# Optimization experiments

Hardware: AMD Instinct MI355X
Metric: run time of the kernel (lower is better)

Reference implementation:

```python
import jax, jax.numpy as jnp
import numpy as np

IN_DIM = 128
SLOT_SIZE = 64
NUM_SLOTS = 8
NUM_ITERS = 3
MLP_HDIM = 128
EPSILON = 1e-08


def _layernorm(x, g, b, eps=1e-5):
    m = jnp.mean(x, axis=-1, keepdims=True)
    v = jnp.mean((x - m) ** 2, axis=-1, keepdims=True)
    return (x - m) * jax.lax.rsqrt(v + eps) * g + b


def setup_inputs() -> dict:
    key = jax.random.key(0)
    ks = jax.random.split(key, 16)
    H, D, K, M = SLOT_SIZE, IN_DIM, NUM_SLOTS, MLP_HDIM
    x = jax.random.normal(ks[0], (32, 4096, D), dtype=jnp.float32)
    noise = jax.random.normal(ks[1], (32, K, H), dtype=jnp.float32)
    s = lambda k, shape, fan_in: jax.random.normal(k, shape, jnp.float32) * (1.0 / np.sqrt(fan_in))
    return {
        'x': x,
        'noise': noise,
        'Wq': s(ks[2], (H, H), H),            # project_q (no bias)
        'Wk': s(ks[3], (H, D), D),            # project_k
        'Wv': s(ks[4], (H, D), D),            # project_v
        'ln_in_g': jnp.ones((D,), jnp.float32), 'ln_in_b': jnp.zeros((D,), jnp.float32),
        'ln_sl_g': jnp.ones((H,), jnp.float32), 'ln_sl_b': jnp.zeros((H,), jnp.float32),
        'ln_mlp_g': jnp.ones((H,), jnp.float32), 'ln_mlp_b': jnp.zeros((H,), jnp.float32),
        'gru_w_ih': s(ks[5], (3 * H, H), H),  # PyTorch GRUCell weight_ih (r,z,n)
        'gru_w_hh': s(ks[6], (3 * H, H), H),
        'gru_b_ih': jnp.zeros((3 * H,), jnp.float32),
        'gru_b_hh': jnp.zeros((3 * H,), jnp.float32),
        'mlp_w1': s(ks[7], (M, H), H), 'mlp_b1': jnp.zeros((M,), jnp.float32),
        'mlp_w2': s(ks[8], (H, M), M), 'mlp_b2': jnp.zeros((H,), jnp.float32),
        'slots_mu': jnp.tile(jnp.linspace(-1.0, 1.0, K, dtype=jnp.float32)[None, :, None], (1, 1, H)),
        'slots_logsigma': jnp.full((1, K, H), -1.0, dtype=jnp.float32),
    }


def reference(x, noise, Wq, Wk, Wv, ln_in_g, ln_in_b, ln_sl_g, ln_sl_b,
              ln_mlp_g, ln_mlp_b, gru_w_ih, gru_w_hh, gru_b_ih, gru_b_hh,
              mlp_w1, mlp_b1, mlp_w2, mlp_b2, slots_mu, slots_logsigma):
    B = x.shape[0]
    H, K = SLOT_SIZE, NUM_SLOTS
    xn = _layernorm(x, ln_in_g, ln_in_b)
    k = jnp.einsum('bnd,hd->bnh', xn, Wk)  # [B,N,H]
    v = jnp.einsum('bnd,hd->bnh', xn, Wv)

    scale = jax.nn.softplus(slots_logsigma) + 1e-05
    slots = slots_mu + scale * noise  # rsample, broadcast over batch -> [B,K,H]

    def step(slots):
        slots_prev = slots
        s = _layernorm(slots, ln_sl_g, ln_sl_b)
        q = jnp.einsum('bkh,gh->bkg', s, Wq)  # [B,K,H]
        scores = (H ** -0.5) * jnp.einsum('bnh,bkh->bnk', k, q)
        attn = jax.nn.softmax(scores, axis=-1) + EPSILON  # softmax over slots
        attn = attn / jnp.sum(attn, axis=1, keepdims=True)  # normalize over inputs
        updates = jnp.einsum('bnk,bnh->bkh', attn, v)
        # PyTorch GRUCell: gates ordered (r, z, n)
        u = updates.reshape(-1, H)
        h = slots_prev.reshape(-1, H)
        gx = u @ gru_w_ih.T + gru_b_ih
        gh = h @ gru_w_hh.T + gru_b_hh
        xr, xz, xn_ = jnp.split(gx, 3, axis=-1)
        hr, hz, hn = jnp.split(gh, 3, axis=-1)
        r = jax.nn.sigmoid(xr + hr)
        z = jax.nn.sigmoid(xz + hz)
        n = jnp.tanh(xn_ + r * hn)
        slots = ((1.0 - z) * n + z * h).reshape(B, K, H)
        slots = _layernorm(slots, ln_mlp_g, ln_mlp_b)
        mlp_out = jax.nn.relu(slots @ mlp_w1.T + mlp_b1) @ mlp_w2.T + mlp_b2
        return slots + mlp_out

    for _ in range(NUM_ITERS):
        slots = step(slots)
    return slots
```

## Files before the change

kernel.cpp:

```cpp
#include <hip/hip_runtime.h>

typedef __attribute__((ext_vector_type(8))) short s16x8;
typedef __attribute__((ext_vector_type(4))) float f32x4;

#define DEV static __device__ __forceinline__

DEV float b2f(unsigned short u){
  unsigned int i = ((unsigned int)u) << 16;
  float f; __builtin_memcpy(&f, &i, 4); return f;
}
DEV unsigned short f2b(float f){
  unsigned int i; __builtin_memcpy(&i, &f, 4);
  i = i + 0x7fffu + ((i >> 16) & 1u);
  return (unsigned short)(i >> 16);
}
DEV f32x4 mfma16(s16x8 a, s16x8 b, f32x4 c){
  return __builtin_amdgcn_mfma_f32_16x16x32_bf16(a, b, c, 0, 0, 0);
}
DEV s16x8 ld8f(const float* p){
  const float4* q4 = (const float4*)p;
  float4 a = q4[0], b = q4[1];
  s16x8 r;
  r[0]=(short)f2b(a.x); r[1]=(short)f2b(a.y); r[2]=(short)f2b(a.z); r[3]=(short)f2b(a.w);
  r[4]=(short)f2b(b.x); r[5]=(short)f2b(b.y); r[6]=(short)f2b(b.z); r[7]=(short)f2b(b.w);
  return r;
}

template<int C> DEV float dpp_addstep(float x){
  int y = __builtin_amdgcn_update_dpp(0, __builtin_bit_cast(int, x), C, 0xF, 0xF, true);
  return x + __builtin_bit_cast(float, y);
}
DEV float rsum16(float v){
  v = dpp_addstep<0xB1>(v);
  v = dpp_addstep<0x4E>(v);
  v = dpp_addstep<0x141>(v);
  v = dpp_addstep<0x140>(v);
  return v;
}

__global__ __launch_bounds__(256) void k_wpack(
    const float* __restrict__ Wk, const float* __restrict__ Wv,
    const float* __restrict__ wih, const float* __restrict__ whh,
    const float* __restrict__ w1, const float* __restrict__ w2,
    const float* __restrict__ Wq,
    unsigned short* __restrict__ wkb, unsigned short* __restrict__ wvb,
    unsigned short* __restrict__ wall)
{
  int t = blockIdx.x * 256 + threadIdx.x;
  int off = t * 4;
  const float* src; unsigned short* dst;
  if      (off <  8192){ src = Wk  + off;         dst = wkb  + off; }
  else if (off < 16384){ src = Wv  + off -  8192; dst = wvb  + off - 8192; }
  else if (off < 28672){ src = wih + off - 16384; dst = wall + off - 16384; }
  else if (off < 40960){ src = whh + off - 28672; dst = wall + off - 16384; }
  else if (off < 49152){ src = w1  + off - 40960; dst = wall + off - 16384; }
  else if (off < 57344){ src = w2  + off - 49152; dst = wall + off - 16384; }
  else                 { src = Wq  + off - 57344; dst = wall + off - 16384; }
  float4 v = *(const float4*)src;
  ushort4 o;
  o.x = f2b(v.x); o.y = f2b(v.y); o.z = f2b(v.z); o.w = f2b(v.w);
  *(ushort4*)dst = o;
}

__global__ __launch_bounds__(256, 4) void k_lnkv5(
    const float* __restrict__ x,
    const unsigned short* __restrict__ wkb,
    const unsigned short* __restrict__ wvb,
    const float* __restrict__ lg,
    const float* __restrict__ lb,
    unsigned short* __restrict__ kg,
    unsigned short* __restrict__ vt,
    const float* __restrict__ noise,
    const float* __restrict__ mu,
    const float* __restrict__ lsg,
    const float* __restrict__ gsl,
    const float* __restrict__ bsl,
    const float* __restrict__ Wq,
    float* __restrict__ slots,
    unsigned short* __restrict__ qws)
{
  __shared__ __align__(16) unsigned int xs[128 * 68];
  const int tid = threadIdx.x;
  const int w = tid >> 6, ln = tid & 63;
  const int m16 = ln & 15, q = ln >> 4;

  if (blockIdx.x >= 1024){
    unsigned short* st = (unsigned short*)xs;
    float (*redS)[4] = (float(*)[4])((char*)xs + 2304);
    float (*redQ)[4] = (float(*)[4])((char*)xs + 2560);
    const int bi = blockIdx.x - 1024;
    const int r0 = bi * 16;
    const int cw = w*16 + m16;

    float sl[4], s1[4], s2[4];
    #pragma unroll
    for (int rr = 0; rr < 4; ++rr){
      int row = r0 + q*4 + rr;
      int k = row & 7;
      float v = mu[k*64 + cw] + (log1pf(expf(lsg[k*64 + cw])) + 1e-5f) * noise[row*64 + cw];
      sl[rr] = v;
      slots[row*64 + cw] = v;
      s1[rr] = v; s2[rr] = v*v;
    }
    #pragma unroll
    for (int m = 1; m < 16; m <<= 1){
      #pragma unroll
      for (int rr = 0; rr < 4; ++rr){
        s1[rr] += __shfl_xor(s1[rr], m);
        s2[rr] += __shfl_xor(s2[rr], m);
      }
    }
    if (m16 == 0){
      #pragma unroll
      for (int rr = 0; rr < 4; ++rr){ redS[q*4+rr][w] = s1[rr]; redQ[q*4+rr][w] = s2[rr]; }
    }
    __syncthreads();
    {
      const float gs = gsl[cw], bs = bsl[cw];
      #pragma unroll
      for (int rr = 0; rr < 4; ++rr){
        f32x4 aS = *(const f32x4*)redS[q*4+rr];
        f32x4 aQ = *(const f32x4*)redQ[q*4+rr];
        float tS = aS[0]+aS[1]+aS[2]+aS[3];
        float tQ = aQ[0]+aQ[1]+aQ[2]+aQ[3];
        float mean = tS*(1.f/64.f);
        float var  = tQ*(1.f/64.f) - mean*mean;
        float rs = rsqrtf(var + 1e-5f);
        float sq = (sl[rr] - mean)*rs*gs + bs;
        st[(q*4+rr)*72 + cw] = f2b(sq);
      }
    }
    __syncthreads();
    {
      f32x4 acc = {0,0,0,0};
      #pragma unroll
      for (int ks = 0; ks < 2; ++ks){
        s16x8 a = *(const s16x8*)(st + m16*72 + ks*32 + q*8);
        acc = mfma16(a, ld8f(Wq + cw*64 + ks*32 + q*8), acc);
      }
      #pragma unroll
      for (int rr = 0; rr < 4; ++rr){
        int row = r0 + q*4 + rr;
        int bb_ = row >> 3, kk = row & 7;
        qws[(bb_*16 + kk)*64 + cw] = f2b(acc[rr] * 0.125f);
      }
      int b0 = bi * 2;
      ((unsigned int*)(qws + (b0*16 + 8)*64))[tid] = 0u;
      ((unsigned int*)(qws + ((b0+1)*16 + 8)*64))[tid] = 0u;
    }
    return;
  }

  const int b = blockIdx.x >> 5;
  const int nbase = (blockIdx.x & 31) << 7;
  const long rowg0 = (long)b * 4096 + nbase;

  {
    const int c = m16;
    const float4 gA = *(const float4*)(lg + c*4);
    const float4 gB = *(const float4*)(lg + 64 + c*4);
    const float4 bA = *(const float4*)(lb + c*4);
    const float4 bB = *(const float4*)(lb + 64 + c*4);
    const float* base = x + (rowg0 + w*32 + q)*128;

    float4 va[2], vb[2];
    va[0] = *(const float4*)(base + c*4);
    vb[0] = *(const float4*)(base + 64 + c*4);
    #pragma unroll
    for (int p = 0; p < 8; ++p){
      const int cur = p & 1, nxt = cur ^ 1;
      if (p < 7){
        va[nxt] = *(const float4*)(base + (p+1)*512 + c*4);
        vb[nxt] = *(const float4*)(base + (p+1)*512 + 64 + c*4);
      }
      float4 u = va[cur], t = vb[cur];
      float s1 = (u.x + u.y) + (u.z + u.w) + (t.x + t.y) + (t.z + t.w);
      float s2 = (u.x*u.x + u.y*u.y) + (u.z*u.z + u.w*u.w)
               + (t.x*t.x + t.y*t.y) + (t.z*t.z + t.w*t.w);
      s1 = rsum16(s1);
      s2 = rsum16(s2);
      float mean = s1 * (1.f/128.f);
      float var  = s2 * (1.f/128.f) - mean*mean;
      float rs = rsqrtf(var + 1e-5f);
      float y0 = (u.x - mean)*rs*gA.x + bA.x;
      float y1 = (u.y - mean)*rs*gA.y + bA.y;
      float y2 = (u.z - mean)*rs*gA.z + bA.z;
      float y3 = (u.w - mean)*rs*gA.w + bA.w;
      float y4 = (t.x - mean)*rs*gB.x + bB.x;
      float y5 = (t.y - mean)*rs*gB.y + bB.y;
      float y6 = (t.z - mean)*rs*gB.z + bB.z;
      float y7 = (t.w - mean)*rs*gB.w + bB.w;
      uint2 pkA, pkB;
      pkA.x = (unsigned int)f2b(y0) | ((unsigned int)f2b(y1) << 16);
      pkA.y = (unsigned int)f2b(y2) | ((unsigned int)f2b(y3) << 16);
      pkB.x = (unsigned int)f2b(y4) | ((unsigned int)f2b(y5) << 16);
      pkB.y = (unsigned int)f2b(y6) | ((unsigned int)f2b(y7) << 16);
      const int r = w*32 + p*4 + q;
      *(uint2*)&xs[r*68 + c*2] = pkA;
      *(uint2*)&xs[r*68 + 32 + c*2] = pkB;
    }
  }

  s16x8 bw[4][4];
  #pragma unroll
  for (int t = 0; t < 4; ++t)
    #pragma unroll
    for (int kb = 0; kb < 4; ++kb)
      bw[kb][t] = *(const s16x8*)(wkb + (t*16 + m16)*128 + kb*32 + q*8);

  __syncthreads();

  const f32x4 zf = {0.f, 0.f, 0.f, 0.f};

  #pragma unroll
  for (int mi = 0; mi < 2; ++mi){
    int n0 = (w*2 + mi) * 16;
    f32x4 acc[4];
    #pragma unroll
    for (int t = 0; t < 4; ++t) acc[t] = zf;
    #pragma unroll
    for (int kb = 0; kb < 4; ++kb){
      s16x8 af = *(const s16x8*)((const unsigned short*)(xs + (n0 + m16)*68) + kb*32 + q*8);
      #pragma unroll
      for (int t = 0; t < 4; ++t)
        acc[t] = mfma16(af, bw[kb][t], acc[t]);
    }
    #pragma unroll
    for (int t = 0; t < 4; ++t){
      int h = t*16 + m16;
      #pragma unroll
      for (int rr = 0; rr < 4; ++rr){
        long n = rowg0 + n0 + q*4 + rr;
        kg[n*64 + h] = f2b(acc[t][rr]);
      }
    }
  }

  #pragma unroll
  for (int t = 0; t < 4; ++t)
    #pragma unroll
    for (int kb = 0; kb < 4; ++kb)
      bw[kb][t] = *(const s16x8*)(wvb + (t*16 + m16)*128 + kb*32 + q*8);

  #pragma unroll
  for (int mi = 0; mi < 2; ++mi){
    int n0 = (w*2 + mi) * 16;
    f32x4 acc[4];
    #pragma unroll
    for (int t = 0; t < 4; ++t) acc[t] = zf;
    #pragma unroll
    for (int kb = 0; kb < 4; ++kb){
      s16x8 af = *(const s16x8*)((const unsigned short*)(xs + (n0 + m16)*68) + kb*32 + q*8);
      #pragma unroll
      for (int t = 0; t < 4; ++t)
        acc[t] = mfma16(af, bw[kb][t], acc[t]);
    }
    #pragma unroll
    for (int t = 0; t < 4; ++t){
      int h = t*16 + m16;
      unsigned int p0 = (unsigned int)f2b(acc[t][0]) | ((unsigned int)f2b(acc[t][1]) << 16);
      unsigned int p1 = (unsigned int)f2b(acc[t][2]) | ((unsigned int)f2b(acc[t][3]) << 16);
      uint2 pv; pv.x = p0; pv.y = p1;
      long off = ((long)b*64 + h)*4096 + nbase + n0 + q*4;
      *(uint2*)(vt + off) = pv;
    }
  }
}

__global__ __launch_bounds__(256) void k_attn3(
    const unsigned short* __restrict__ kg,
    const unsigned short* __restrict__ vt,
    const unsigned short* __restrict__ qws,
    const unsigned short* __restrict__ wall,
    const float* __restrict__ bih, const float* __restrict__ bhh,
    const float* __restrict__ b1p, const float* __restrict__ b2p,
    const float* __restrict__ gmlp, const float* __restrict__ bmlp,
    const float* __restrict__ gsl, const float* __restrict__ bsl,
    const float* __restrict__ Up_in, const float* __restrict__ Sp_in,
    float* __restrict__ Up_out, float* __restrict__ Sp_out,
    const float* __restrict__ slin, float* __restrict__ slout,
    int it)
{
  __shared__ float sc[256*17];
  __shared__ unsigned short aT[16*264];
  __shared__ unsigned short ut[16*72], ht[16*72], st[16*72], hid[16*136];
  __shared__ unsigned short qloc[16*72];
  __shared__ __align__(16) float redS[16][4];
  __shared__ __align__(16) float redQ[16][4];

  const int tid = threadIdx.x;
  const int w = tid >> 6, ln = tid & 63;
  const int m16 = ln & 15, q = ln >> 4;
  const int b = blockIdx.x >> 4;
  const int tile = blockIdx.x & 15;
  const int nbase = tile << 8;

  for (int i = tid; i < 8*264; i += 256) aT[8*264 + i] = 0;
  if (tid < 128){
    int row = 8 + (tid >> 4), c = (tid & 15)*4;
    ushort4 z4 = {0,0,0,0};
    *(ushort4*)&qloc[row*72 + c] = z4;
  }

  if (it == 0){
    if (tid < 128){
      int row = tid >> 4, c = (tid & 15)*4;
      *(ushort4*)&qloc[row*72 + c] = *(const ushort4*)(qws + (b*16 + row)*64 + c);
    }
  } else {
    const int r0 = (b >> 1) * 16;
    const int cw = w*16 + m16;
    const unsigned short* wihb = wall;
    const unsigned short* whhb = wall + 12288;
    const unsigned short* w1b  = wall + 24576;
    const unsigned short* w2b  = wall + 32768;
    const unsigned short* wqb  = wall + 40960;

    #pragma unroll
    for (int p = 0; p < 4; ++p){
      int row = p*4 + w;
      int g = r0 + row;
      int bb = g >> 3, sl = g & 7;
      const float* up  = Up_in + ((bb*16)*8 + sl)*64 + ln;
      const float* spp = Sp_in + (bb*16)*8 + sl;
      float usum = 0.f, ssum = 0.f;
      #pragma unroll
      for (int t = 0; t < 16; ++t){
        usum += up[t*512];
        ssum += spp[t*8];
      }
      ut[row*72 + ln] = f2b(usum / ssum);
      ht[row*72 + ln] = f2b(slin[g*64 + ln]);
    }
    __syncthreads();

    f32x4 axr = {0,0,0,0}, axz = {0,0,0,0}, axn = {0,0,0,0};
    f32x4 ahr = {0,0,0,0}, ahz = {0,0,0,0}, ahn = {0,0,0,0};
    #pragma unroll
    for (int ks = 0; ks < 2; ++ks){
      s16x8 au = *(const s16x8*)(ut + m16*72 + ks*32 + q*8);
      s16x8 ah = *(const s16x8*)(ht + m16*72 + ks*32 + q*8);
      axr = mfma16(au, *(const s16x8*)(wihb + (      cw)*64 + ks*32 + q*8), axr);
      axz = mfma16(au, *(const s16x8*)(wihb + ( 64 + cw)*64 + ks*32 + q*8), axz);
      axn = mfma16(au, *(const s16x8*)(wihb + (128 + cw)*64 + ks*32 + q*8), axn);
      ahr = mfma16(ah, *(const s16x8*)(whhb + (      cw)*64 + ks*32 + q*8), ahr);
      ahz = mfma16(ah, *(const s16x8*)(whhb + ( 64 + cw)*64 + ks*32 + q*8), ahz);
      ahn = mfma16(ah, *(const s16x8*)(whhb + (128 + cw)*64 + ks*32 + q*8), ahn);
    }
    const float bxr = bih[cw], bxz = bih[64+cw], bxn = bih[128+cw];
    const float bhr = bhh[cw], bhz = bhh[64+cw], bhn = bhh[128+cw];
    float sp[4];
    #pragma unroll
    for (int rr = 0; rr < 4; ++rr){
      float xr = axr[rr] + bxr, xz = axz[rr] + bxz, xnv = axn[rr] + bxn;
      float hr = ahr[rr] + bhr, hz = ahz[rr] + bhz, hn = ahn[rr] + bhn;
      float rg = 1.f / (1.f + expf(-(xr + hr)));
      float zg = 1.f / (1.f + expf(-(xz + hz)));
      float ng = tanhf(xnv + rg*hn);
      float hv = b2f(ht[(q*4 + rr)*72 + cw]);
      sp[rr] = (1.f - zg)*ng + zg*hv;
    }

    float s1[4], s2[4];
    #pragma unroll
    for (int rr = 0; rr < 4; ++rr){ s1[rr] = sp[rr]; s2[rr] = sp[rr]*sp[rr]; }
    #pragma unroll
    for (int m = 1; m < 16; m <<= 1){
      #pragma unroll
      for (int rr = 0; rr < 4; ++rr){
        s1[rr] += __shfl_xor(s1[rr], m);
        s2[rr] += __shfl_xor(s2[rr], m);
      }
    }
    if (m16 == 0){
      #pragma unroll
      for (int rr = 0; rr < 4; ++rr){ redS[q*4+rr][w] = s1[rr]; redQ[q*4+rr][w] = s2[rr]; }
    }
    __syncthreads();
    float sl_[4];
    {
      const float gm = gmlp[cw], bm = bmlp[cw];
      #pragma unroll
      for (int rr = 0; rr < 4; ++rr){
        f32x4 aS = *(const f32x4*)redS[q*4+rr];
        f32x4 aQ = *(const f32x4*)redQ[q*4+rr];
        float tS = aS[0]+aS[1]+aS[2]+aS[3];
        float tQ = aQ[0]+aQ[1]+aQ[2]+aQ[3];
        float mean = tS*(1.f/64.f);
        float var  = tQ*(1.f/64.f) - mean*mean;
        float rs = rsqrtf(var + 1e-5f);
        sl_[rr] = (sp[rr] - mean)*rs*gm + bm;
        st[(q*4+rr)*72 + cw] = f2b(sl_[rr]);
      }
    }
    __syncthreads();

    #pragma unroll
    for (int t2 = 0; t2 < 2; ++t2){
      int nt = w*2 + t2;
      int col = nt*16 + m16;
      f32x4 acc = {0,0,0,0};
      #pragma unroll
      for (int ks = 0; ks < 2; ++ks){
        s16x8 a = *(const s16x8*)(st + m16*72 + ks*32 + q*8);
        acc = mfma16(a, *(const s16x8*)(w1b + col*64 + ks*32 + q*8), acc);
      }
      float bb = b1p[col];
      #pragma unroll
      for (int rr = 0; rr < 4; ++rr)
        hid[(q*4+rr)*136 + col] = f2b(fmaxf(acc[rr] + bb, 0.f));
    }
    __syncthreads();

    float snew[4];
    {
      f32x4 acc = {0,0,0,0};
      #pragma unroll
      for (int ks = 0; ks < 4; ++ks){
        s16x8 a = *(const s16x8*)(hid + m16*136 + ks*32 + q*8);
        acc = mfma16(a, *(const s16x8*)(w2b + cw*128 + ks*32 + q*8), acc);
      }
      float bb = b2p[cw];
      #pragma unroll
      for (int rr = 0; rr < 4; ++rr){
        snew[rr] = sl_[rr] + acc[rr] + bb;
        if ((blockIdx.x & 31) == 0)
          slout[(r0 + q*4 + rr)*64 + cw] = snew[rr];
      }
    }

    #pragma unroll
    for (int rr = 0; rr < 4; ++rr){ s1[rr] = snew[rr]; s2[rr] = snew[rr]*snew[rr]; }
    #pragma unroll
    for (int m = 1; m < 16; m <<= 1){
      #pragma unroll
      for (int rr = 0; rr < 4; ++rr){
        s1[rr] += __shfl_xor(s1[rr], m);
        s2[rr] += __shfl_xor(s2[rr], m);
      }
    }
    __syncthreads();
    if (m16 == 0){
      #pragma unroll
      for (int rr = 0; rr < 4; ++rr){ redS[q*4+rr][w] = s1[rr]; redQ[q*4+rr][w] = s2[rr]; }
    }
    __syncthreads();
    {
      const float gs = gsl[cw], bs = bsl[cw];
      #pragma unroll
      for (int rr = 0; rr < 4; ++rr){
        f32x4 aS = *(const f32x4*)redS[q*4+rr];
        f32x4 aQ = *(const f32x4*)redQ[q*4+rr];
        float tS = aS[0]+aS[1]+aS[2]+aS[3];
        float tQ = aQ[0]+aQ[1]+aQ[2]+aQ[3];
        float mean = tS*(1.f/64.f);
        float var  = tQ*(1.f/64.f) - mean*mean;
        float rs = rsqrtf(var + 1e-5f);
        float sq = (snew[rr] - mean)*rs*gs + bs;
        st[(q*4+rr)*72 + cw] = f2b(sq);
      }
    }
    __syncthreads();
    {
      f32x4 acc = {0,0,0,0};
      #pragma unroll
      for (int ks = 0; ks < 2; ++ks){
        s16x8 a = *(const s16x8*)(st + m16*72 + ks*32 + q*8);
        acc = mfma16(a, *(const s16x8*)(wqb + cw*64 + ks*32 + q*8), acc);
      }
      #pragma unroll
      for (int rr = 0; rr < 4; ++rr){
        int rloc = q*4 + rr;
        if ((rloc >> 3) == (b & 1))
          qloc[(rloc & 7)*72 + cw] = f2b(acc[rr] * 0.125f);
      }
    }
  }
  __syncthreads();

  s16x8 bq[2];
  #pragma unroll
  for (int ks = 0; ks < 2; ++ks)
    bq[ks] = *(const s16x8*)(qloc + m16*72 + ks*32 + q*8);

  #pragma unroll
  for (int mi = 0; mi < 4; ++mi){
    int n0 = (w*4 + mi)*16;
    f32x4 acc = {0.f, 0.f, 0.f, 0.f};
    #pragma unroll
    for (int ks = 0; ks < 2; ++ks){
      s16x8 af = *(const s16x8*)(kg + ((long)b*4096 + nbase + n0 + m16)*64 + ks*32 + q*8);
      acc = mfma16(af, bq[ks], acc);
    }
    #pragma unroll
    for (int rr = 0; rr < 4; ++rr)
      sc[(n0 + q*4 + rr)*17 + m16] = acc[rr];
  }
  __syncthreads();

  {
    int r = tid;
    float a8[8];
    float mx = -1e30f;
    #pragma unroll
    for (int j = 0; j < 8; ++j){ a8[j] = sc[r*17 + j]; mx = fmaxf(mx, a8[j]); }
    float ssum = 0.f;
    #pragma unroll
    for (int j = 0; j < 8; ++j){ a8[j] = expf(a8[j] - mx); ssum += a8[j]; }
    float inv = 1.f/ssum;
    #pragma unroll
    for (int j = 0; j < 8; ++j)
      aT[j*264 + r] = f2b(a8[j]*inv + 1e-8f);
  }
  __syncthreads();

  {
    int j = tid >> 5, c = tid & 31;
    float p = 0.f;
    #pragma unroll
    for (int i = 0; i < 8; ++i) p += b2f(aT[j*264 + c + 32*i]);
    #pragma unroll
    for (int m = 16; m >= 1; m >>= 1) p += __shfl_xor(p, m);
    if ((tid & 31) == 0) Sp_out[(b*16 + tile)*8 + j] = p;
  }

  {
    f32x4 acc = {0.f, 0.f, 0.f, 0.f};
    #pragma unroll
    for (int ks = 0; ks < 8; ++ks){
      s16x8 af = *(const s16x8*)(aT + m16*264 + ks*32 + q*8);
      s16x8 bf = *(const s16x8*)(vt + ((long)b*64 + w*16 + m16)*4096 + nbase + ks*32 + q*8);
      acc = mfma16(af, bf, acc);
    }
    float* ub = Up_out + ((b*16 + tile)*8)*64 + w*16 + m16;
    #pragma unroll
    for (int rr = 0; rr < 4; ++rr){
      int slot = q*4 + rr;
      if (slot < 8)
        ub[slot*64] = acc[rr];
    }
  }
}

__global__ __launch_bounds__(256) void k_gru2(
    const float* __restrict__ Up, const float* __restrict__ Sp,
    const float* __restrict__ slots,
    const float* __restrict__ wih, const float* __restrict__ whh,
    const float* __restrict__ bih, const float* __restrict__ bhh,
    const float* __restrict__ w1, const float* __restrict__ b1p,
    const float* __restrict__ w2, const float* __restrict__ b2p,
    const float* __restrict__ gmlp, const float* __restrict__ bmlp,
    float* __restrict__ outp)
{
  __shared__ unsigned short ut[16*72], ht[16*72], st[16*72], hid[16*136];
  __shared__ __align__(16) float redS[16][4];
  __shared__ __align__(16) float redQ[16][4];
  const int tid = threadIdx.x;
  const int w = tid >> 6, ln = tid & 63;
  const int m16 = ln & 15, q = ln >> 4;
  const int r0 = blockIdx.x * 16;
  const int cw = w*16 + m16;

  #pragma unroll
  for (int p = 0; p < 4; ++p){
    int row = p*4 + w;
    int g = r0 + row;
    int bb = g >> 3, sl = g & 7;
    const float* up  = Up + ((bb*16)*8 + sl)*64 + ln;
    const float* spp = Sp + (bb*16)*8 + sl;
    float usum = 0.f, ssum = 0.f;
    #pragma unroll
    for (int t = 0; t < 16; ++t){
      usum += up[t*512];
      ssum += spp[t*8];
    }
    ut[row*72 + ln] = f2b(usum / ssum);
    ht[row*72 + ln] = f2b(slots[g*64 + ln]);
  }
  __syncthreads();

  f32x4 axr = {0,0,0,0}, axz = {0,0,0,0}, axn = {0,0,0,0};
  f32x4 ahr = {0,0,0,0}, ahz = {0,0,0,0}, ahn = {0,0,0,0};
  #pragma unroll
  for (int ks = 0; ks < 2; ++ks){
    s16x8 au = *(const s16x8*)(ut + m16*72 + ks*32 + q*8);
    s16x8 ah = *(const s16x8*)(ht + m16*72 + ks*32 + q*8);
    axr = mfma16(au, ld8f(wih + (      cw)*64 + ks*32 + q*8), axr);
    axz = mfma16(au, ld8f(wih + ( 64 + cw)*64 + ks*32 + q*8), axz);
    axn = mfma16(au, ld8f(wih + (128 + cw)*64 + ks*32 + q*8), axn);
    ahr = mfma16(ah, ld8f(whh + (      cw)*64 + ks*32 + q*8), ahr);
    ahz = mfma16(ah, ld8f(whh + ( 64 + cw)*64 + ks*32 + q*8), ahz);
    ahn = mfma16(ah, ld8f(whh + (128 + cw)*64 + ks*32 + q*8), ahn);
  }
  const float bxr = bih[cw], bxz = bih[64+cw], bxn = bih[128+cw];
  const float bhr = bhh[cw], bhz = bhh[64+cw], bhn = bhh[128+cw];
  float sp[4];
  #pragma unroll
  for (int rr = 0; rr < 4; ++rr){
    float xr = axr[rr] + bxr, xz = axz[rr] + bxz, xnv = axn[rr] + bxn;
    float hr = ahr[rr] + bhr, hz = ahz[rr] + bhz, hn = ahn[rr] + bhn;
    float rg = 1.f / (1.f + expf(-(xr + hr)));
    float zg = 1.f / (1.f + expf(-(xz + hz)));
    float ng = tanhf(xnv + rg*hn);
    float hv = b2f(ht[(q*4 + rr)*72 + cw]);
    sp[rr] = (1.f - zg)*ng + zg*hv;
  }

  float s1[4], s2[4];
  #pragma unroll
  for (int rr = 0; rr < 4; ++rr){ s1[rr] = sp[rr]; s2[rr] = sp[rr]*sp[rr]; }
  #pragma unroll
  for (int m = 1; m < 16; m <<= 1){
    #pragma unroll
    for (int rr = 0; rr < 4; ++rr){
      s1[rr] += __shfl_xor(s1[rr], m);
      s2[rr] += __shfl_xor(s2[rr], m);
    }
  }
  if (m16 == 0){
    #pragma unroll
    for (int rr = 0; rr < 4; ++rr){ redS[q*4+rr][w] = s1[rr]; redQ[q*4+rr][w] = s2[rr]; }
  }
  __syncthreads();
  float sl_[4];
  {
    const float gm = gmlp[cw], bm = bmlp[cw];
    #pragma unroll
    for (int rr = 0; rr < 4; ++rr){
      f32x4 aS = *(const f32x4*)redS[q*4+rr];
      f32x4 aQ = *(const f32x4*)redQ[q*4+rr];
      float tS = aS[0]+aS[1]+aS[2]+aS[3];
      float tQ = aQ[0]+aQ[1]+aQ[2]+aQ[3];
      float mean = tS*(1.f/64.f);
      float var  = tQ*(1.f/64.f) - mean*mean;
      float rs = rsqrtf(var + 1e-5f);
      sl_[rr] = (sp[rr] - mean)*rs*gm + bm;
      st[(q*4+rr)*72 + cw] = f2b(sl_[rr]);
    }
  }
  __syncthreads();

  #pragma unroll
  for (int t2 = 0; t2 < 2; ++t2){
    int nt = w*2 + t2;
    int col = nt*16 + m16;
    f32x4 acc = {0,0,0,0};
    #pragma unroll
    for (int ks = 0; ks < 2; ++ks){
      s16x8 a = *(const s16x8*)(st + m16*72 + ks*32 + q*8);
      acc = mfma16(a, ld8f(w1 + col*64 + ks*32 + q*8), acc);
    }
    float bb = b1p[col];
    #pragma unroll
    for (int rr = 0; rr < 4; ++rr)
      hid[(q*4+rr)*136 + col] = f2b(fmaxf(acc[rr] + bb, 0.f));
  }
  __syncthreads();

  {
    f32x4 acc = {0,0,0,0};
    #pragma unroll
    for (int ks = 0; ks < 4; ++ks){
      s16x8 a = *(const s16x8*)(hid + m16*136 + ks*32 + q*8);
      acc = mfma16(a, ld8f(w2 + cw*128 + ks*32 + q*8), acc);
    }
    float bb = b2p[cw];
    #pragma unroll
    for (int rr = 0; rr < 4; ++rr){
      int row = r0 + q*4 + rr;
      outp[row*64 + cw] = sl_[rr] + acc[rr] + bb;
    }
  }
}

extern "C" void kernel_launch(void* const* d_in, const int* in_sizes, int n_in,
                              void* d_out, int out_size, void* d_ws, size_t ws_size,
                              hipStream_t stream)
{
  const float* x    = (const float*)d_in[0];
  const float* noise= (const float*)d_in[1];
  const float* Wq   = (const float*)d_in[2];
  const float* Wk   = (const float*)d_in[3];
  const float* Wv   = (const float*)d_in[4];
  const float* ling = (const float*)d_in[5];
  const float* linb = (const float*)d_in[6];
  const float* gsl  = (const float*)d_in[7];
  const float* bsl  = (const float*)d_in[8];
  const float* gmlp = (const float*)d_in[9];
  const float* bmlp = (const float*)d_in[10];
  const float* wih  = (const float*)d_in[11];
  const float* whh  = (const float*)d_in[12];
  const float* bih  = (const float*)d_in[13];
  const float* bhh  = (const float*)d_in[14];
  const float* w1   = (const float*)d_in[15];
  const float* b1p  = (const float*)d_in[16];
  const float* w2   = (const float*)d_in[17];
  const float* b2p  = (const float*)d_in[18];
  const float* mu   = (const float*)d_in[19];
  const float* lsg  = (const float*)d_in[20];

  char* ws = (char*)d_ws;
  unsigned short* kg   = (unsigned short*)(ws);
  unsigned short* vt   = (unsigned short*)(ws + 16777216);
  char* base = ws + 33554432;
  unsigned short* qws  = (unsigned short*)(base);
  float* slotsA        = (float*)(base + 65536);
  float* slotsB        = (float*)(base + 131072);
  float* slotsC        = (float*)(base + 196608);
  float* UA            = (float*)(base + 262144);
  float* UB            = (float*)(base + 1310720);
  float* SA            = (float*)(base + 2359296);
  float* SB            = (float*)(base + 2375680);
  unsigned short* wkb  = (unsigned short*)(base + 2392064);
  unsigned short* wvb  = (unsigned short*)(base + 2408448);
  unsigned short* wall = (unsigned short*)(base + 2424832);
  float* outp          = (float*)d_out;

  hipLaunchKernelGGL(k_wpack, dim3(60), dim3(256), 0, stream,
                     Wk, Wv, wih, whh, w1, w2, Wq, wkb, wvb, wall);
  hipLaunchKernelGGL(k_lnkv5, dim3(1040), dim3(256), 0, stream,
                     x, wkb, wvb, ling, linb, kg, vt,
                     noise, mu, lsg, gsl, bsl, Wq, slotsA, qws);
  hipLaunchKernelGGL(k_attn3, dim3(512), dim3(256), 0, stream,
                     kg, vt, qws, wall, bih, bhh, b1p, b2p, gmlp, bmlp, gsl, bsl,
                     UA, SA, UA, SA, slotsA, slotsA, 0);
  hipLaunchKernelGGL(k_attn3, dim3(512), dim3(256), 0, stream,
                     kg, vt, qws, wall, bih, bhh, b1p, b2p, gmlp, bmlp, gsl, bsl,
                     UA, SA, UB, SB, slotsA, slotsB, 1);
  hipLaunchKernelGGL(k_attn3, dim3(512), dim3(256), 0, stream,
                     kg, vt, qws, wall, bih, bhh, b1p, b2p, gmlp, bmlp, gsl, bsl,
                     UB, SB, UA, SA, slotsB, slotsC, 2);
  hipLaunchKernelGGL(k_gru2, dim3(16), dim3(256), 0, stream, UA, SA, slotsC,
                     wih, whh, bih, bhh, w1, b1p, w2, b2p, gmlp, bmlp, outp);
  (void)in_sizes; (void)n_in; (void)out_size; (void)ws_size;
}
```

Before: 203.2 us.

## Prefetch K/V tiles at kernel start and use DPP-style row reductions

Moves the global loads of the key and value MFMA fragments to the very start of the attention kernel, so they are in flight while the slot GRU/MLP/LayerNorm recomputation runs. Replaces the shuffle-xor reduction loops with an rsum16 helper, likely based on cross-lane DPP/permute ops. Adds a second pair of reduction buffers so one __syncthreads can be dropped. Holding the prefetched fragments costs roughly 32 extra VGPRs, which may reduce occupancy. rsum16 is not defined in the visible hunks.

```diff
diff --git a/kernel.cpp b/kernel.cpp
--- a/kernel.cpp
+++ b/kernel.cpp
@@ -100,15 +100,8 @@
       float v = mu[k*64 + cw] + (log1pf(expf(lsg[k*64 + cw])) + 1e-5f) * noise[row*64 + cw];
       sl[rr] = v;
       slots[row*64 + cw] = v;
-      s1[rr] = v; s2[rr] = v*v;
-    }
-    #pragma unroll
-    for (int m = 1; m < 16; m <<= 1){
-      #pragma unroll
-      for (int rr = 0; rr < 4; ++rr){
-        s1[rr] += __shfl_xor(s1[rr], m);
-        s2[rr] += __shfl_xor(s2[rr], m);
-      }
+      s1[rr] = rsum16(v);
+      s2[rr] = rsum16(v*v);
     }
     if (m16 == 0){
       #pragma unroll
@@ -287,6 +280,8 @@
   __shared__ unsigned short qloc[16*72];
   __shared__ __align__(16) float redS[16][4];
   __shared__ __align__(16) float redQ[16][4];
+  __shared__ __align__(16) float redS2[16][4];
+  __shared__ __align__(16) float redQ2[16][4];
 
   const int tid = threadIdx.x;
   const int w = tid >> 6, ln = tid & 63;
@@ -294,6 +289,23 @@
   const int b = blockIdx.x >> 4;
   const int tile = blockIdx.x & 15;
   const int nbase = tile << 8;
+
+  s16x8 afp[4];
+  #pragma unroll
+  for (int mi = 0; mi < 4; ++mi){
+    int n0 = (w*4 + mi)*16;
+    afp[mi] = *(const s16x8*)(kg + ((long)b*4096 + nbase + n0 + m16)*64 + q*8);
+  }
+  s16x8 afp2[4];
+  #pragma unroll
+  for (int mi = 0; mi < 4; ++mi){
+    int n0 = (w*4 + mi)*16;
+    afp2[mi] = *(const s16x8*)(kg + ((long)b*4096 + nbase + n0 + m16)*64 + 32 + q*8);
+  }
+  s16x8 vtp[8];
+  #pragma unroll
+  for (int ks = 0; ks < 8; ++ks)
+    vtp[ks] = *(const s16x8*)(vt + ((long)b*64 + w*16 + m16)*4096 + nbase + ks*32 + q*8);
 
   for (int i = tid; i < 8*264; i += 256) aT[8*264 + i] = 0;
   if (tid < 128){
@@ -363,14 +375,9 @@
 
     float s1[4], s2[4];
     #pragma unroll
-    for (int rr = 0; rr < 4; ++rr){ s1[rr] = sp[rr]; s2[rr] = sp[rr]*sp[rr]; }
-    #pragma unroll
-    for (int m = 1; m < 16; m <<= 1){
-      #pragma unroll
-      for (int rr = 0; rr < 4; ++rr){
-        s1[rr] += __shfl_xor(s1[rr], m);
-        s2[rr] += __shfl_xor(s2[rr], m);
-      }
+    for (int rr = 0; rr < 4; ++rr){
+      s1[rr] = rsum16(sp[rr]);
+      s2[rr] = rsum16(sp[rr]*sp[rr]);
     }
     if (m16 == 0){
       #pragma unroll
@@ -430,27 +437,21 @@
     }
 
     #pragma unroll
-    for (int rr = 0; rr < 4; ++rr){ s1[rr] = snew[rr]; s2[rr] = snew[rr]*snew[rr]; }
-    #pragma unroll
-    for (int m = 1; m < 16; m <<= 1){
-      #pragma unroll
-      for (int rr = 0; rr < 4; ++rr){
-        s1[rr] += __shfl_xor(s1[rr], m);
-        s2[rr] += __shfl_xor(s2[rr], m);
-      }
-    }
-    __syncthreads();
+    for (int rr = 0; rr < 4; ++rr){
+      s1[rr] = rsum16(snew[rr]);
+      s2[rr] = rsum16(snew[rr]*snew[rr]);
+    }
     if (m16 == 0){
       #pragma unroll
-      for (int rr = 0; rr < 4; ++rr){ redS[q*4+rr][w] = s1[rr]; redQ[q*4+rr][w] = s2[rr]; }
+      for (int rr = 0; rr < 4; ++rr){ redS2[q*4+rr][w] = s1[rr]; redQ2[q*4+rr][w] = s2[rr]; }
     }
     __syncthreads();
     {
       const float gs = gsl[cw], bs = bsl[cw];
       #pragma unroll
       for (int rr = 0; rr < 4; ++rr){
-        f32x4 aS = *(const f32x4*)redS[q*4+rr];
-        f32x4 aQ = *(const f32x4*)redQ[q*4+rr];
+        f32x4 aS = *(const f32x4*)redS2[q*4+rr];
+        f32x4 aQ = *(const f32x4*)redQ2[q*4+rr];
         float tS = aS[0]+aS[1]+aS[2]+aS[3];
         float tQ = aQ[0]+aQ[1]+aQ[2]+aQ[3];
         float mean = tS*(1.f/64.f);
@@ -487,11 +488,8 @@
   for (int mi = 0; mi < 4; ++mi){
     int n0 = (w*4 + mi)*16;
     f32x4 acc = {0.f, 0.f, 0.f, 0.f};
-    #pragma unroll
-    for (int ks = 0; ks < 2; ++ks){
-      s16x8 af = *(const s16x8*)(kg + ((long)b*4096 + nbase + n0 + m16)*64 + ks*32 + q*8);
-      acc = mfma16(af, bq[ks], acc);
-    }
+    acc = mfma16(afp[mi],  bq[0], acc);
+    acc = mfma16(afp2[mi], bq[1], acc);
     #pragma unroll
     for (int rr = 0; rr < 4; ++rr)
       sc[(n0 + q*4 + rr)*17 + m16] = acc[rr];
@@ -519,8 +517,8 @@
     float p = 0.f;
     #pragma unroll
     for (int i = 0; i < 8; ++i) p += b2f(aT[j*264 + c + 32*i]);
-    #pragma unroll
-    for (int m = 16; m >= 1; m >>= 1) p += __shfl_xor(p, m);
+    p = rsum16(p);
+    p += __shfl_xor(p, 16);
     if ((tid & 31) == 0) Sp_out[(b*16 + tile)*8 + j] = p;
   }
 
@@ -529,8 +527,7 @@
     #pragma unroll
     for (int ks = 0; ks < 8; ++ks){
       s16x8 af = *(const s16x8*)(aT + m16*264 + ks*32 + q*8);
-      s16x8 bf = *(const s16x8*)(vt + ((long)b*64 + w*16 + m16)*4096 + nbase + ks*32 + q*8);
-      acc = mfma16(af, bf, acc);
+      acc = mfma16(af, vtp[ks], acc);
     }
     float* ub = Up_out + ((b*16 + tile)*8)*64 + w*16 + m16;
     #pragma unroll
@@ -608,14 +605,9 @@
 
   float s1[4], s2[4];
   #pragma unroll
-  for (int rr = 0; rr < 4; ++rr){ s1[rr] = sp[rr]; s2[rr] = sp[rr]*sp[rr]; }
-  #pragma unroll
-  for (int m = 1; m < 16; m <<= 1){
-    #pragma unroll
-    for (int rr = 0; rr < 4; ++rr){
-      s1[rr] += __shfl_xor(s1[rr], m);
-      s2[rr] += __shfl_xor(s2[rr], m);
-    }
+  for (int rr = 0; rr < 4; ++rr){
+    s1[rr] = rsum16(sp[rr]);
+    s2[rr] = rsum16(sp[rr]*sp[rr]);
   }
   if (m16 == 0){
     #pragma unroll
```

Result: no change. 201.9 us (-0.6%).
